# Kernel tuning notes

Measured on AMD Instinct MI355X. Metric: run time of the kernel, lower is better.

## Reference

```python
import jax, jax.numpy as jnp
import numpy as np
import math

HID = 128
NH = 8
HD = HID // NH
NL = 3
CLIP = 10.0
EPS = 1e-5

def _ln(x, g, b):
    mu = jnp.mean(x, axis=-1, keepdims=True)
    var = jnp.var(x, axis=-1, keepdims=True)
    return (x - mu) * jax.lax.rsqrt(var + EPS) * g + b

def _layer(h, e_bias1, e_gate2, g1, b1, wh, g2, b2, w1, w2):
    B, N, _ = h.shape
    h_in = h
    hn = _ln(h, g1, b1)
    qkv = hn @ wh                                   # (B,N,3H)
    q, k, v = jnp.split(qkv, 3, axis=-1)
    q = q.reshape(B, N, NH, HD).transpose(0, 2, 1, 3)  # (B,nh,N,hd)
    k = k.reshape(B, N, NH, HD).transpose(0, 2, 1, 3)
    v = v.reshape(B, N, NH, HD).transpose(0, 2, 1, 3)
    att = jnp.einsum('bhid,bhjd->bhij', q, k) * (1.0 / math.sqrt(HD))
    att = jax.nn.softmax(att + e_bias1, axis=-1) * e_gate2
    y = jnp.einsum('bhij,bhjd->bhid', att, v)
    y = y.transpose(0, 2, 1, 3).reshape(B, N, HID)
    z = _ln(y + h_in, g2, b2)
    mlp = jax.nn.relu(z @ w1) @ w2
    return mlp + y

def setup_inputs() -> dict:
    key = jax.random.key(0)
    ks = jax.random.split(key, 9)
    d = {
        'node_features': jax.random.normal(ks[0], (16, 256, 2), jnp.float32),
        'edge_features': jax.random.normal(ks[1], (16, 256, 256, 1), jnp.float32),
        'Wn': jax.random.normal(ks[2], (2, HID), jnp.float32) * 0.5,
        'We_in': jax.random.normal(ks[3], (1, HID), jnp.float32) * 0.1,
        'ln1_g': jnp.ones((NL, HID), jnp.float32),
        'ln1_b': jnp.zeros((NL, HID), jnp.float32),
        'Wh': jax.random.normal(ks[4], (NL, HID, 3 * HID), jnp.float32) * (1.0 / math.sqrt(HID)),
        'We': jax.random.normal(ks[5], (NL, HID, 2 * NH), jnp.float32) * (1.0 / math.sqrt(HID)),
        'ln2_g': jnp.ones((NL, HID), jnp.float32),
        'ln2_b': jnp.zeros((NL, HID), jnp.float32),
        'W1': jax.random.normal(ks[6], (NL, HID, 4 * HID), jnp.float32) * (1.0 / math.sqrt(HID)),
        'W2': jax.random.normal(ks[7], (NL, 4 * HID, HID), jnp.float32) * (1.0 / math.sqrt(4 * HID)),
        'Wdec': jax.random.normal(ks[8], (HID, 1), jnp.float32) * (1.0 / math.sqrt(HID)),
    }
    return d

def reference(node_features, edge_features, Wn, We_in, ln1_g, ln1_b, Wh, We, ln2_g, ln2_b, W1, W2, Wdec):
    h = node_features @ Wn                              # (B,N,H)
    e = edge_features @ We_in                           # (B,N,N,H)
    for i in range(NL):
        ee = e @ We[i]                                  # (B,N,N,2*nh)
        ee = ee.transpose(0, 3, 1, 2)                   # (B,2*nh,N,N)
        e1, e2 = ee[:, :NH], ee[:, NH:]
        h = _layer(h, e1, e2, ln1_g[i], ln1_b[i], Wh[i], ln2_g[i], ln2_b[i], W1[i], W2[i])
    out = h @ Wdec                                      # (B,N,1)
    out = CLIP * jnp.tanh(out / math.sqrt(HID))
    return out
```

## Files before the change

kernel.cpp:

```cpp
#include <hip/hip_runtime.h>
#include <math.h>

#define HID 128
#define NHEAD 8
#define NL 3
#define NS 256
#define ROWS 4096

typedef __attribute__((ext_vector_type(8))) short bf16x8;
typedef __attribute__((ext_vector_type(4))) float f32x4;

__device__ __forceinline__ float us2f(unsigned short s) { return __uint_as_float(((unsigned)s) << 16); }
__device__ __forceinline__ unsigned short f2b(float f) {
    unsigned u = __float_as_uint(f);
    return (unsigned short)((u + 0x7fff + ((u >> 16) & 1)) >> 16);
}

__global__ __launch_bounds__(256) void k_prep(
    const float* __restrict__ Wh, const float* __restrict__ W1, const float* __restrict__ W2,
    const float* __restrict__ We_in, const float* __restrict__ We,
    unsigned short* __restrict__ WhH, unsigned short* __restrict__ WhL,
    unsigned short* __restrict__ W1H, unsigned short* __restrict__ W1L,
    unsigned short* __restrict__ W2H, unsigned short* __restrict__ W2L,
    float* __restrict__ sbuf)
{
    int b = blockIdx.x, t = threadIdx.x;
    if (b == 528) {
        if (t < NL * 2 * NHEAD) {
            int l = t / (2 * NHEAD), j = t % (2 * NHEAD);
            float acc = 0.f;
            for (int c = 0; c < HID; ++c)
                acc += We_in[c] * We[(long)(l * HID + c) * (2 * NHEAD) + j];
            sbuf[t] = acc;
        }
        return;
    }
    const float* S; unsigned short *OH, *OL; int K, N, kt, nt;
    if (b < 144) {
        int l = b / 48, rem = b % 48; kt = rem & 3; nt = rem >> 2; K = 128; N = 384;
        S = Wh + (long)l * 128 * 384; OH = WhH + (long)l * 384 * 128; OL = WhL + (long)l * 384 * 128;
    } else if (b < 336) {
        int b2 = b - 144; int l = b2 / 64, rem = b2 % 64; kt = rem & 3; nt = rem >> 2; K = 128; N = 512;
        S = W1 + (long)l * 128 * 512; OH = W1H + (long)l * 512 * 128; OL = W1L + (long)l * 512 * 128;
    } else {
        int b2 = b - 336; int l = b2 / 64, rem = b2 % 64; kt = rem & 15; nt = rem >> 4; K = 512; N = 128;
        S = W2 + (long)l * 512 * 128; OH = W2H + (long)l * 128 * 512; OL = W2L + (long)l * 128 * 512;
    }
    __shared__ float sm[32][33];
    int i0 = t >> 5, j = t & 31;
#pragma unroll
    for (int p = 0; p < 4; ++p) {
        int i = i0 + p * 8;
        sm[i][j] = S[(long)(kt * 32 + i) * N + nt * 32 + j];
    }
    __syncthreads();
#pragma unroll
    for (int p = 0; p < 4; ++p) {
        int n = i0 + p * 8;
        float v = sm[j][n];
        unsigned short hh = f2b(v);
        long o = (long)(nt * 32 + n) * K + kt * 32 + j;
        OH[o] = hh; OL[o] = f2b(v - us2f(hh));
    }
}

__global__ __launch_bounds__(256) void k_embln(
    const float* __restrict__ nf, const float* __restrict__ Wn,
    const float* __restrict__ g, const float* __restrict__ b,
    float* __restrict__ h, unsigned short* __restrict__ oh, unsigned short* __restrict__ ol)
{
    int w = threadIdx.x >> 6, lane = threadIdx.x & 63;
    int row = blockIdx.x * 4 + w;
    int base = row * HID;
    float n0 = nf[2 * row], n1 = nf[2 * row + 1];
    float v0 = n0 * Wn[lane]      + n1 * Wn[HID + lane];
    float v1 = n0 * Wn[64 + lane] + n1 * Wn[HID + 64 + lane];
    h[base + lane] = v0; h[base + 64 + lane] = v1;
    float s = v0 + v1, s2 = v0 * v0 + v1 * v1;
#pragma unroll
    for (int o = 32; o; o >>= 1) { s += __shfl_xor(s, o); s2 += __shfl_xor(s2, o); }
    float mu  = s * (1.f / HID);
    float var = s2 * (1.f / HID) - mu * mu;
    float inv = rsqrtf(var + 1e-5f);
    float o0 = (v0 - mu) * inv * g[lane]      + b[lane];
    float o1 = (v1 - mu) * inv * g[64 + lane] + b[64 + lane];
    unsigned short h0 = f2b(o0), h1 = f2b(o1);
    oh[base + lane] = h0;       ol[base + lane] = f2b(o0 - us2f(h0));
    oh[base + 64 + lane] = h1;  ol[base + 64 + lane] = f2b(o1 - us2f(h1));
}

__global__ __launch_bounds__(256) void k_ln(const float* __restrict__ x,
                                            const float* __restrict__ x2,
                                            const float* __restrict__ g,
                                            const float* __restrict__ b,
                                            unsigned short* __restrict__ oh,
                                            unsigned short* __restrict__ ol) {
    int w = threadIdx.x >> 6, lane = threadIdx.x & 63;
    int row = blockIdx.x * 4 + w;
    int base = row * HID;
    float v0 = x[base + lane] + x2[base + lane];
    float v1 = x[base + 64 + lane] + x2[base + 64 + lane];
    float s = v0 + v1, s2 = v0 * v0 + v1 * v1;
#pragma unroll
    for (int o = 32; o; o >>= 1) { s += __shfl_xor(s, o); s2 += __shfl_xor(s2, o); }
    float mu  = s * (1.f / HID);
    float var = s2 * (1.f / HID) - mu * mu;
    float inv = rsqrtf(var + 1e-5f);
    float o0 = (v0 - mu) * inv * g[lane]      + b[lane];
    float o1 = (v1 - mu) * inv * g[64 + lane] + b[64 + lane];
    unsigned short h0 = f2b(o0), h1 = f2b(o1);
    oh[base + lane] = h0;       ol[base + lane] = f2b(o0 - us2f(h0));
    oh[base + 64 + lane] = h1;  ol[base + 64 + lane] = f2b(o1 - us2f(h1));
}

__global__ __launch_bounds__(256, 4) void k_gemm(
    const unsigned short* __restrict__ Ah, const unsigned short* __restrict__ Al,
    const unsigned short* __restrict__ WH, const unsigned short* __restrict__ WL,
    float* __restrict__ Cf, unsigned short* __restrict__ Ch, unsigned short* __restrict__ Cl,
    int Nc, int K, int mode)
{
    __shared__ unsigned short sAh[64 * 72], sAl[64 * 72], sWh[64 * 72], sWl[64 * 72];
    int t = threadIdx.x;
    int row0 = blockIdx.y * 64, col0 = blockIdx.x * 64;
    int w = t >> 6, lane = t & 63;
    int m = lane & 15, quad = lane >> 4;
    f32x4 acc[4];
#pragma unroll
    for (int i = 0; i < 4; ++i) acc[i] = (f32x4){0.f, 0.f, 0.f, 0.f};

    for (int ks = 0; ks < K; ks += 64) {
        if (ks) __syncthreads();
        int r = t >> 3, ck = t & 7;
#pragma unroll
        for (int p = 0; p < 2; ++p) {
            int rr = r + p * 32;
            long ga = (long)(row0 + rr) * K + ks + ck * 8;
            long wa = (long)(col0 + rr) * K + ks + ck * 8;
            *(uint4*)&sAh[rr * 72 + ck * 8] = *(const uint4*)&Ah[ga];
            *(uint4*)&sAl[rr * 72 + ck * 8] = *(const uint4*)&Al[ga];
            *(uint4*)&sWh[rr * 72 + ck * 8] = *(const uint4*)&WH[wa];
            *(uint4*)&sWl[rr * 72 + ck * 8] = *(const uint4*)&WL[wa];
        }
        __syncthreads();
#pragma unroll
        for (int c = 0; c < 2; ++c) {
            bf16x8 ah = *(const bf16x8*)&sAh[(w * 16 + m) * 72 + c * 32 + quad * 8];
            bf16x8 al = *(const bf16x8*)&sAl[(w * 16 + m) * 72 + c * 32 + quad * 8];
#pragma unroll
            for (int nt = 0; nt < 4; ++nt) {
                bf16x8 wh = *(const bf16x8*)&sWh[(nt * 16 + m) * 72 + c * 32 + quad * 8];
                bf16x8 wl = *(const bf16x8*)&sWl[(nt * 16 + m) * 72 + c * 32 + quad * 8];
                acc[nt] = __builtin_amdgcn_mfma_f32_16x16x32_bf16(ah, wh, acc[nt], 0, 0, 0);
                acc[nt] = __builtin_amdgcn_mfma_f32_16x16x32_bf16(ah, wl, acc[nt], 0, 0, 0);
                acc[nt] = __builtin_amdgcn_mfma_f32_16x16x32_bf16(al, wh, acc[nt], 0, 0, 0);
            }
        }
    }
#pragma unroll
    for (int nt = 0; nt < 4; ++nt) {
#pragma unroll
        for (int r = 0; r < 4; ++r) {
            int row = row0 + w * 16 + quad * 4 + r;
            int col = col0 + nt * 16 + m;
            float v = acc[nt][r];
            if (mode == 0) {
                Cf[(long)row * Nc + col] = v;
            } else {
                v = fmaxf(v, 0.f);
                unsigned short hh = f2b(v);
                Ch[(long)row * Nc + col] = hh;
                Cl[(long)row * Nc + col] = f2b(v - us2f(hh));
            }
        }
    }
}

__global__ __launch_bounds__(256, 3) void k_w2ln(
    const unsigned short* __restrict__ Ah, const unsigned short* __restrict__ Al,
    const unsigned short* __restrict__ WH, const unsigned short* __restrict__ WL,
    const float* __restrict__ yres, float* __restrict__ hout,
    const float* __restrict__ g, const float* __restrict__ b,
    unsigned short* __restrict__ oh, unsigned short* __restrict__ ol)
{
    __shared__ unsigned short sA[2][16 * 72];
    __shared__ unsigned short sW[2][128 * 72];
    int t = threadIdx.x;
    int row0 = blockIdx.x * 16;
    int w = t >> 6, lane = t & 63;
    int m = lane & 15, quad = lane >> 4;
    f32x4 acc[2];
    acc[0] = (f32x4){0.f,0.f,0.f,0.f}; acc[1] = (f32x4){0.f,0.f,0.f,0.f};

    for (int ks = 0; ks < 512; ks += 64) {
        if (ks) __syncthreads();
        {
            int pl = t >> 7, tt = t & 127;
            int r = tt >> 3, ck = tt & 7;
            const unsigned short* src = pl ? Al : Ah;
            *(uint4*)&sA[pl][r * 72 + ck * 8] = *(const uint4*)&src[(long)(row0 + r) * 512 + ks + ck * 8];
        }
        {
            int r0 = t >> 3, ck = t & 7;
#pragma unroll
            for (int p = 0; p < 4; ++p) {
                int n = r0 + p * 32;
                *(uint4*)&sW[0][n * 72 + ck * 8] = *(const uint4*)&WH[(long)n * 512 + ks + ck * 8];
                *(uint4*)&sW[1][n * 72 + ck * 8] = *(const uint4*)&WL[(long)n * 512 + ks + ck * 8];
            }
        }
        __syncthreads();
#pragma unroll
        for (int c = 0; c < 2; ++c) {
            bf16x8 ah = *(const bf16x8*)&sA[0][m * 72 + c * 32 + quad * 8];
            bf16x8 al = *(const bf16x8*)&sA[1][m * 72 + c * 32 + quad * 8];
#pragma unroll
            for (int nt = 0; nt < 2; ++nt) {
                int n = w * 32 + nt * 16 + m;
                bf16x8 wh = *(const bf16x8*)&sW[0][n * 72 + c * 32 + quad * 8];
                bf16x8 wl = *(const bf16x8*)&sW[1][n * 72 + c * 32 + quad * 8];
                acc[nt] = __builtin_amdgcn_mfma_f32_16x16x32_bf16(ah, wh, acc[nt], 0, 0, 0);
                acc[nt] = __builtin_amdgcn_mfma_f32_16x16x32_bf16(ah, wl, acc[nt], 0, 0, 0);
                acc[nt] = __builtin_amdgcn_mfma_f32_16x16x32_bf16(al, wh, acc[nt], 0, 0, 0);
            }
        }
    }
    __syncthreads();
    float* ht = (float*)&sW[0][0];
#pragma unroll
    for (int nt = 0; nt < 2; ++nt) {
#pragma unroll
        for (int r = 0; r < 4; ++r) {
            int row = quad * 4 + r;
            int col = w * 32 + nt * 16 + m;
            float v = acc[nt][r] + yres[(long)(row0 + row) * HID + col];
            hout[(long)(row0 + row) * HID + col] = v;
            ht[row * 132 + col] = v;
        }
    }
    __syncthreads();
    if (g) {
        int row = t >> 4, sub = t & 15;
        float v[8];
        *(float4*)&v[0] = *(const float4*)&ht[row * 132 + sub * 8];
        *(float4*)&v[4] = *(const float4*)&ht[row * 132 + sub * 8 + 4];
        float s = 0.f, s2 = 0.f;
#pragma unroll
        for (int j = 0; j < 8; ++j) { s += v[j]; s2 += v[j] * v[j]; }
        s  += __shfl_xor(s, 1);  s  += __shfl_xor(s, 2);  s  += __shfl_xor(s, 4);  s  += __shfl_xor(s, 8);
        s2 += __shfl_xor(s2, 1); s2 += __shfl_xor(s2, 2); s2 += __shfl_xor(s2, 4); s2 += __shfl_xor(s2, 8);
        float mu  = s * (1.f / HID);
        float var = s2 * (1.f / HID) - mu * mu;
        float inv = rsqrtf(var + 1e-5f);
        long base = (long)(row0 + row) * HID + sub * 8;
#pragma unroll
        for (int j = 0; j < 8; ++j) {
            int c = sub * 8 + j;
            float o = (v[j] - mu) * inv * g[c] + b[c];
            unsigned short hh = f2b(o);
            oh[base + j] = hh; ol[base + j] = f2b(o - us2f(hh));
        }
    }
}

__global__ __launch_bounds__(256) void k_attn(const float* __restrict__ qkv,
                                              const float* __restrict__ ef,
                                              const float* __restrict__ sbuf,
                                              int layer,
                                              float* __restrict__ y) {
    __shared__ float Ks[NS][20];
    __shared__ float Vt[16][NS + 4];
    __shared__ float Pb[4][4][NS];
    int bid = blockIdx.x;
    int q4 = bid & 3, hh = (bid >> 2) & 7, bb = bid >> 5;
    int t = threadIdx.x;
    {
        const float* kr = qkv + ((long)(bb * NS + t)) * 384 + HID + hh * 16;
        *(float4*)&Ks[t][0]  = *(const float4*)kr;
        *(float4*)&Ks[t][4]  = *(const float4*)(kr + 4);
        *(float4*)&Ks[t][8]  = *(const float4*)(kr + 8);
        *(float4*)&Ks[t][12] = *(const float4*)(kr + 12);
        const float* vr = kr + HID;
        float vv[16];
        *(float4*)&vv[0]  = *(const float4*)vr;
        *(float4*)&vv[4]  = *(const float4*)(vr + 4);
        *(float4*)&vv[8]  = *(const float4*)(vr + 8);
        *(float4*)&vv[12] = *(const float4*)(vr + 12);
#pragma unroll
        for (int d = 0; d < 16; ++d) Vt[d][t] = vv[d];
    }
    __syncthreads();
    int w = t >> 6, lane = t & 63;
    float s1  = sbuf[layer * 16 + hh];
    float s2g = sbuf[layer * 16 + NHEAD + hh];
    int part = lane >> 4, dd = lane & 15;
    for (int it = 0; it < 4; ++it) {
        int r0 = q4 * 64 + w * 16 + it * 4;
        float q[4][16];
#pragma unroll
        for (int rr = 0; rr < 4; ++rr) {
            const float* qr = qkv + ((long)(bb * NS + r0 + rr)) * 384 + hh * 16;
            *(float4*)&q[rr][0]  = *(const float4*)qr;
            *(float4*)&q[rr][4]  = *(const float4*)(qr + 4);
            *(float4*)&q[rr][8]  = *(const float4*)(qr + 8);
            *(float4*)&q[rr][12] = *(const float4*)(qr + 12);
        }
        float sc[4][4];
#pragma unroll
        for (int i = 0; i < 4; ++i) {
            int c = i * 64 + lane;
            float kk[16];
            *(float4*)&kk[0]  = *(const float4*)&Ks[c][0];
            *(float4*)&kk[4]  = *(const float4*)&Ks[c][4];
            *(float4*)&kk[8]  = *(const float4*)&Ks[c][8];
            *(float4*)&kk[12] = *(const float4*)&Ks[c][12];
#pragma unroll
            for (int rr = 0; rr < 4; ++rr) {
                float d0 = 0.f;
#pragma unroll
                for (int d = 0; d < 16; ++d) d0 += q[rr][d] * kk[d];
                sc[rr][i] = d0;
            }
        }
#pragma unroll
        for (int rr = 0; rr < 4; ++rr) {
            long eb = ((long)(bb * NS + r0 + rr)) * NS;
            float e0 = ef[eb + lane],       e1 = ef[eb + 64 + lane];
            float e2 = ef[eb + 128 + lane], e3 = ef[eb + 192 + lane];
            float x0 = sc[rr][0] * 0.25f + e0 * s1;
            float x1 = sc[rr][1] * 0.25f + e1 * s1;
            float x2 = sc[rr][2] * 0.25f + e2 * s1;
            float x3 = sc[rr][3] * 0.25f + e3 * s1;
            float m = fmaxf(fmaxf(x0, x1), fmaxf(x2, x3));
#pragma unroll
            for (int o = 32; o; o >>= 1) m = fmaxf(m, __shfl_xor(m, o));
            float p0 = __expf(x0 - m), p1 = __expf(x1 - m);
            float p2 = __expf(x2 - m), p3 = __expf(x3 - m);
            float sum = p0 + p1 + p2 + p3;
#pragma unroll
            for (int o = 32; o; o >>= 1) sum += __shfl_xor(sum, o);
            float inv = s2g / sum;
            Pb[w][rr][lane]       = p0 * inv * e0;
            Pb[w][rr][64 + lane]  = p1 * inv * e1;
            Pb[w][rr][128 + lane] = p2 * inv * e2;
            Pb[w][rr][192 + lane] = p3 * inv * e3;
        }
        float a0 = 0.f, a1 = 0.f, a2 = 0.f, a3 = 0.f;
#pragma unroll
        for (int ii = 0; ii < 16; ++ii) {
            int c = part * 64 + ((ii + part * 4) & 15) * 4;
            float4 vv = *(const float4*)&Vt[dd][c];
            float4 p;
            p = *(const float4*)&Pb[w][0][c]; a0 += vv.x*p.x + vv.y*p.y + vv.z*p.z + vv.w*p.w;
            p = *(const float4*)&Pb[w][1][c]; a1 += vv.x*p.x + vv.y*p.y + vv.z*p.z + vv.w*p.w;
            p = *(const float4*)&Pb[w][2][c]; a2 += vv.x*p.x + vv.y*p.y + vv.z*p.z + vv.w*p.w;
            p = *(const float4*)&Pb[w][3][c]; a3 += vv.x*p.x + vv.y*p.y + vv.z*p.z + vv.w*p.w;
        }
        a0 += __shfl_xor(a0, 16); a0 += __shfl_xor(a0, 32);
        a1 += __shfl_xor(a1, 16); a1 += __shfl_xor(a1, 32);
        a2 += __shfl_xor(a2, 16); a2 += __shfl_xor(a2, 32);
        a3 += __shfl_xor(a3, 16); a3 += __shfl_xor(a3, 32);
        if (lane < 16) {
            y[((long)(bb * NS + r0 + 0)) * HID + hh * 16 + dd] = a0;
            y[((long)(bb * NS + r0 + 1)) * HID + hh * 16 + dd] = a1;
            y[((long)(bb * NS + r0 + 2)) * HID + hh * 16 + dd] = a2;
            y[((long)(bb * NS + r0 + 3)) * HID + hh * 16 + dd] = a3;
        }
    }
}

__global__ __launch_bounds__(256) void k_dec(const float* __restrict__ h,
                                             const float* __restrict__ Wdec,
                                             float* __restrict__ out) {
    int w = threadIdx.x >> 6, lane = threadIdx.x & 63;
    int row = blockIdx.x * 4 + w;
    float a = h[(long)row * HID + lane] * Wdec[lane]
            + h[(long)row * HID + 64 + lane] * Wdec[64 + lane];
#pragma unroll
    for (int o = 32; o; o >>= 1) a += __shfl_xor(a, o);
    if (lane == 0) out[row] = 10.f * tanhf(a * 0.08838834764831845f);
}

extern "C" void kernel_launch(void* const* d_in, const int* in_sizes, int n_in,
                              void* d_out, int out_size, void* d_ws, size_t ws_size,
                              hipStream_t stream) {
    const float* nf    = (const float*)d_in[0];
    const float* ef    = (const float*)d_in[1];
    const float* Wn    = (const float*)d_in[2];
    const float* We_in = (const float*)d_in[3];
    const float* ln1g  = (const float*)d_in[4];
    const float* ln1b  = (const float*)d_in[5];
    const float* Wh    = (const float*)d_in[6];
    const float* We    = (const float*)d_in[7];
    const float* ln2g  = (const float*)d_in[8];
    const float* ln2b  = (const float*)d_in[9];
    const float* W1    = (const float*)d_in[10];
    const float* W2    = (const float*)d_in[11];
    const float* Wdec  = (const float*)d_in[12];

    float* ws   = (float*)d_ws;
    float* sbuf = ws;
    float* h    = ws + 64;
    float* y    = h + ROWS * HID;
    float* qkv  = y + ROWS * HID;
    unsigned short* hnH  = (unsigned short*)(qkv + (long)ROWS * 384);
    unsigned short* hnL  = hnH + (long)ROWS * HID;
    unsigned short* hidH = hnL + (long)ROWS * HID;
    unsigned short* hidL = hidH + (long)ROWS * 512;
    unsigned short* WhH  = hidL + (long)ROWS * 512;
    unsigned short* WhL  = WhH + (long)NL * 384 * 128;
    unsigned short* W1H  = WhL + (long)NL * 384 * 128;
    unsigned short* W1L  = W1H + (long)NL * 512 * 128;
    unsigned short* W2H  = W1L + (long)NL * 512 * 128;
    unsigned short* W2L  = W2H + (long)NL * 128 * 512;

    k_prep<<<529, 256, 0, stream>>>(Wh, W1, W2, We_in, We,
                                    WhH, WhL, W1H, W1L, W2H, W2L, sbuf);
    k_embln<<<ROWS / 4, 256, 0, stream>>>(nf, Wn, ln1g, ln1b, h, hnH, hnL);
    for (int l = 0; l < NL; ++l) {
        k_gemm<<<dim3(6, 64), 256, 0, stream>>>(hnH, hnL,
            WhH + (long)l * 384 * 128, WhL + (long)l * 384 * 128,
            qkv, nullptr, nullptr, 384, 128, 0);
        k_attn<<<512, 256, 0, stream>>>(qkv, ef, sbuf, l, y);
        k_ln<<<ROWS / 4, 256, 0, stream>>>(y, h, ln2g + l * HID, ln2b + l * HID, hnH, hnL);
        k_gemm<<<dim3(8, 64), 256, 0, stream>>>(hnH, hnL,
            W1H + (long)l * 512 * 128, W1L + (long)l * 512 * 128,
            nullptr, hidH, hidL, 512, 128, 1);
        int last = (l == NL - 1);
        k_w2ln<<<ROWS / 16, 256, 0, stream>>>(hidH, hidL,
            W2H + (long)l * 128 * 512, W2L + (long)l * 128 * 512,
            y, h,
            last ? nullptr : ln1g + (l + 1) * HID, last ? nullptr : ln1b + (l + 1) * HID,
            hnH, hnL);
    }
    k_dec<<<ROWS / 4, 256, 0, stream>>>(h, Wdec, (float*)d_out);
}
```

Baseline: 243.8 us.

## Fuse LayerNorm into GEMM prologue and decoder into final W2 epilogue

New measurement: 246.9 us. Within noise of the previous version (+1.3%).

```diff
diff --git a/kernel.cpp b/kernel.cpp
--- a/kernel.cpp
+++ b/kernel.cpp
@@ -19,12 +19,19 @@
 __global__ __launch_bounds__(256) void k_prep(
     const float* __restrict__ Wh, const float* __restrict__ W1, const float* __restrict__ W2,
     const float* __restrict__ We_in, const float* __restrict__ We,
+    const float* __restrict__ nf, const float* __restrict__ Wn,
     unsigned short* __restrict__ WhH, unsigned short* __restrict__ WhL,
     unsigned short* __restrict__ W1H, unsigned short* __restrict__ W1L,
     unsigned short* __restrict__ W2H, unsigned short* __restrict__ W2L,
-    float* __restrict__ sbuf)
+    float* __restrict__ sbuf, float* __restrict__ h)
 {
     int b = blockIdx.x, t = threadIdx.x;
+    if (b >= 529) {
+        int idx = (b - 529) * 256 + t;
+        int r = idx >> 7, c = idx & 127;
+        h[idx] = nf[2 * r] * Wn[c] + nf[2 * r + 1] * Wn[HID + c];
+        return;
+    }
     if (b == 528) {
         if (t < NL * 2 * NHEAD) {
             int l = t / (2 * NHEAD), j = t % (2 * NHEAD);
@@ -64,96 +71,78 @@
     }
 }
 
-__global__ __launch_bounds__(256) void k_embln(
-    const float* __restrict__ nf, const float* __restrict__ Wn,
+__global__ __launch_bounds__(256) void k_fgemm(
+    const float* __restrict__ x, const float* __restrict__ x2,
     const float* __restrict__ g, const float* __restrict__ b,
-    float* __restrict__ h, unsigned short* __restrict__ oh, unsigned short* __restrict__ ol)
-{
-    int w = threadIdx.x >> 6, lane = threadIdx.x & 63;
-    int row = blockIdx.x * 4 + w;
-    int base = row * HID;
-    float n0 = nf[2 * row], n1 = nf[2 * row + 1];
-    float v0 = n0 * Wn[lane]      + n1 * Wn[HID + lane];
-    float v1 = n0 * Wn[64 + lane] + n1 * Wn[HID + 64 + lane];
-    h[base + lane] = v0; h[base + 64 + lane] = v1;
-    float s = v0 + v1, s2 = v0 * v0 + v1 * v1;
-#pragma unroll
-    for (int o = 32; o; o >>= 1) { s += __shfl_xor(s, o); s2 += __shfl_xor(s2, o); }
-    float mu  = s * (1.f / HID);
-    float var = s2 * (1.f / HID) - mu * mu;
-    float inv = rsqrtf(var + 1e-5f);
-    float o0 = (v0 - mu) * inv * g[lane]      + b[lane];
-    float o1 = (v1 - mu) * inv * g[64 + lane] + b[64 + lane];
-    unsigned short h0 = f2b(o0), h1 = f2b(o1);
-    oh[base + lane] = h0;       ol[base + lane] = f2b(o0 - us2f(h0));
-    oh[base + 64 + lane] = h1;  ol[base + 64 + lane] = f2b(o1 - us2f(h1));
-}
-
-__global__ __launch_bounds__(256) void k_ln(const float* __restrict__ x,
-                                            const float* __restrict__ x2,
-                                            const float* __restrict__ g,
-                                            const float* __restrict__ b,
-                                            unsigned short* __restrict__ oh,
-                                            unsigned short* __restrict__ ol) {
-    int w = threadIdx.x >> 6, lane = threadIdx.x & 63;
-    int row = blockIdx.x * 4 + w;
-    int base = row * HID;
-    float v0 = x[base + lane] + x2[base + lane];
-    float v1 = x[base + 64 + lane] + x2[base + 64 + lane];
-    float s = v0 + v1, s2 = v0 * v0 + v1 * v1;
-#pragma unroll
-    for (int o = 32; o; o >>= 1) { s += __shfl_xor(s, o); s2 += __shfl_xor(s2, o); }
-    float mu  = s * (1.f / HID);
-    float var = s2 * (1.f / HID) - mu * mu;
-    float inv = rsqrtf(var + 1e-5f);
-    float o0 = (v0 - mu) * inv * g[lane]      + b[lane];
-    float o1 = (v1 - mu) * inv * g[64 + lane] + b[64 + lane];
-    unsigned short h0 = f2b(o0), h1 = f2b(o1);
-    oh[base + lane] = h0;       ol[base + lane] = f2b(o0 - us2f(h0));
-    oh[base + 64 + lane] = h1;  ol[base + 64 + lane] = f2b(o1 - us2f(h1));
-}
-
-__global__ __launch_bounds__(256, 4) void k_gemm(
-    const unsigned short* __restrict__ Ah, const unsigned short* __restrict__ Al,
     const unsigned short* __restrict__ WH, const unsigned short* __restrict__ WL,
     float* __restrict__ Cf, unsigned short* __restrict__ Ch, unsigned short* __restrict__ Cl,
-    int Nc, int K, int mode)
+    int Nc, int mode)
 {
-    __shared__ unsigned short sAh[64 * 72], sAl[64 * 72], sWh[64 * 72], sWl[64 * 72];
+    __shared__ unsigned short sAh[64 * 136], sAl[64 * 136];
+    __shared__ unsigned short sWh[64 * 136], sWl[64 * 136];
     int t = threadIdx.x;
     int row0 = blockIdx.y * 64, col0 = blockIdx.x * 64;
+
+#pragma unroll
+    for (int p = 0; p < 4; ++p) {
+        int rr = (t >> 4) + p * 16, ck = t & 15;
+        *(uint4*)&sWh[rr * 136 + ck * 8] = *(const uint4*)&WH[(long)(col0 + rr) * 128 + ck * 8];
+        *(uint4*)&sWl[rr * 136 + ck * 8] = *(const uint4*)&WL[(long)(col0 + rr) * 128 + ck * 8];
+    }
+#pragma unroll
+    for (int pass = 0; pass < 2; ++pass) {
+        int row = pass * 32 + (t >> 3);
+        int p = t & 7, cb = p * 16;
+        float v[16];
+        const float* xp = x + (long)(row0 + row) * HID + cb;
+#pragma unroll
+        for (int j = 0; j < 16; j += 4) *(float4*)&v[j] = *(const float4*)(xp + j);
+        if (x2) {
+            const float* yp = x2 + (long)(row0 + row) * HID + cb;
+#pragma unroll
+            for (int j = 0; j < 16; j += 4) {
+                float4 r4 = *(const float4*)(yp + j);
+                v[j] += r4.x; v[j+1] += r4.y; v[j+2] += r4.z; v[j+3] += r4.w;
+            }
+        }
+        float s = 0.f, s2 = 0.f;
+#pragma unroll
+        for (int j = 0; j < 16; ++j) { s += v[j]; s2 += v[j] * v[j]; }
+        s  += __shfl_xor(s, 1);  s  += __shfl_xor(s, 2);  s  += __shfl_xor(s, 4);
+        s2 += __shfl_xor(s2, 1); s2 += __shfl_xor(s2, 2); s2 += __shfl_xor(s2, 4);
+        float mu  = s * (1.f / HID);
+        float var = s2 * (1.f / HID) - mu * mu;
+        float inv = rsqrtf(var + 1e-5f);
+        unsigned short hi[16], lo[16];
+#pragma unroll
+        for (int j = 0; j < 16; ++j) {
+            int c = cb + j;
+            float o = (v[j] - mu) * inv * g[c] + b[c];
+            hi[j] = f2b(o); lo[j] = f2b(o - us2f(hi[j]));
+        }
+        *(uint4*)&sAh[row * 136 + cb]     = *(uint4*)&hi[0];
+        *(uint4*)&sAh[row * 136 + cb + 8] = *(uint4*)&hi[8];
+        *(uint4*)&sAl[row * 136 + cb]     = *(uint4*)&lo[0];
+        *(uint4*)&sAl[row * 136 + cb + 8] = *(uint4*)&lo[8];
+    }
+    __syncthreads();
+
     int w = t >> 6, lane = t & 63;
     int m = lane & 15, quad = lane >> 4;
     f32x4 acc[4];
 #pragma unroll
     for (int i = 0; i < 4; ++i) acc[i] = (f32x4){0.f, 0.f, 0.f, 0.f};
-
-    for (int ks = 0; ks < K; ks += 64) {
-        if (ks) __syncthreads();
-        int r = t >> 3, ck = t & 7;
-#pragma unroll
-        for (int p = 0; p < 2; ++p) {
-            int rr = r + p * 32;
-            long ga = (long)(row0 + rr) * K + ks + ck * 8;
-            long wa = (long)(col0 + rr) * K + ks + ck * 8;
-            *(uint4*)&sAh[rr * 72 + ck * 8] = *(const uint4*)&Ah[ga];
-            *(uint4*)&sAl[rr * 72 + ck * 8] = *(const uint4*)&Al[ga];
-            *(uint4*)&sWh[rr * 72 + ck * 8] = *(const uint4*)&WH[wa];
-            *(uint4*)&sWl[rr * 72 + ck * 8] = *(const uint4*)&WL[wa];
-        }
-        __syncthreads();
-#pragma unroll
-        for (int c = 0; c < 2; ++c) {
-            bf16x8 ah = *(const bf16x8*)&sAh[(w * 16 + m) * 72 + c * 32 + quad * 8];
-            bf16x8 al = *(const bf16x8*)&sAl[(w * 16 + m) * 72 + c * 32 + quad * 8];
-#pragma unroll
-            for (int nt = 0; nt < 4; ++nt) {
-                bf16x8 wh = *(const bf16x8*)&sWh[(nt * 16 + m) * 72 + c * 32 + quad * 8];
-                bf16x8 wl = *(const bf16x8*)&sWl[(nt * 16 + m) * 72 + c * 32 + quad * 8];
-                acc[nt] = __builtin_amdgcn_mfma_f32_16x16x32_bf16(ah, wh, acc[nt], 0, 0, 0);
-                acc[nt] = __builtin_amdgcn_mfma_f32_16x16x32_bf16(ah, wl, acc[nt], 0, 0, 0);
-                acc[nt] = __builtin_amdgcn_mfma_f32_16x16x32_bf16(al, wh, acc[nt], 0, 0, 0);
-            }
+#pragma unroll
+    for (int c = 0; c < 4; ++c) {
+        bf16x8 ah = *(const bf16x8*)&sAh[(w * 16 + m) * 136 + c * 32 + quad * 8];
+        bf16x8 al = *(const bf16x8*)&sAl[(w * 16 + m) * 136 + c * 32 + quad * 8];
+#pragma unroll
+        for (int nt = 0; nt < 4; ++nt) {
+            bf16x8 wh = *(const bf16x8*)&sWh[(nt * 16 + m) * 136 + c * 32 + quad * 8];
+            bf16x8 wl = *(const bf16x8*)&sWl[(nt * 16 + m) * 136 + c * 32 + quad * 8];
+            acc[nt] = __builtin_amdgcn_mfma_f32_16x16x32_bf16(ah, wh, acc[nt], 0, 0, 0);
+            acc[nt] = __builtin_amdgcn_mfma_f32_16x16x32_bf16(ah, wl, acc[nt], 0, 0, 0);
+            acc[nt] = __builtin_amdgcn_mfma_f32_16x16x32_bf16(al, wh, acc[nt], 0, 0, 0);
         }
     }
 #pragma unroll
@@ -179,8 +168,7 @@
     const unsigned short* __restrict__ Ah, const unsigned short* __restrict__ Al,
     const unsigned short* __restrict__ WH, const unsigned short* __restrict__ WL,
     const float* __restrict__ yres, float* __restrict__ hout,
-    const float* __restrict__ g, const float* __restrict__ b,
-    unsigned short* __restrict__ oh, unsigned short* __restrict__ ol)
+    const float* __restrict__ Wdec, float* __restrict__ out)
 {
     __shared__ unsigned short sA[2][16 * 72];
     __shared__ unsigned short sW[2][128 * 72];
@@ -238,27 +226,16 @@
         }
     }
     __syncthreads();
-    if (g) {
+    if (Wdec) {
         int row = t >> 4, sub = t & 15;
         float v[8];
         *(float4*)&v[0] = *(const float4*)&ht[row * 132 + sub * 8];
         *(float4*)&v[4] = *(const float4*)&ht[row * 132 + sub * 8 + 4];
-        float s = 0.f, s2 = 0.f;
-#pragma unroll
-        for (int j = 0; j < 8; ++j) { s += v[j]; s2 += v[j] * v[j]; }
-        s  += __shfl_xor(s, 1);  s  += __shfl_xor(s, 2);  s  += __shfl_xor(s, 4);  s  += __shfl_xor(s, 8);
-        s2 += __shfl_xor(s2, 1); s2 += __shfl_xor(s2, 2); s2 += __shfl_xor(s2, 4); s2 += __shfl_xor(s2, 8);
-        float mu  = s * (1.f / HID);
-        float var = s2 * (1.f / HID) - mu * mu;
-        float inv = rsqrtf(var + 1e-5f);
-        long base = (long)(row0 + row) * HID + sub * 8;
-#pragma unroll
-        for (int j = 0; j < 8; ++j) {
-            int c = sub * 8 + j;
-            float o = (v[j] - mu) * inv * g[c] + b[c];
-            unsigned short hh = f2b(o);
-            oh[base + j] = hh; ol[base + j] = f2b(o - us2f(hh));
-        }
+        float a = 0.f;
+#pragma unroll
+        for (int j = 0; j < 8; ++j) a += v[j] * Wdec[sub * 8 + j];
+        a += __shfl_xor(a, 1); a += __shfl_xor(a, 2); a += __shfl_xor(a, 4); a += __shfl_xor(a, 8);
+        if (sub == 0) out[row0 + row] = 10.f * tanhf(a * 0.08838834764831845f);
     }
 }
 
@@ -368,18 +345,6 @@
     }
 }
 
-__global__ __launch_bounds__(256) void k_dec(const float* __restrict__ h,
-                                             const float* __restrict__ Wdec,
-                                             float* __restrict__ out) {
-    int w = threadIdx.x >> 6, lane = threadIdx.x & 63;
-    int row = blockIdx.x * 4 + w;
-    float a = h[(long)row * HID + lane] * Wdec[lane]
-            + h[(long)row * HID + 64 + lane] * Wdec[64 + lane];
-#pragma unroll
-    for (int o = 32; o; o >>= 1) a += __shfl_xor(a, o);
-    if (lane == 0) out[row] = 10.f * tanhf(a * 0.08838834764831845f);
-}
-
 extern "C" void kernel_launch(void* const* d_in, const int* in_sizes, int n_in,
                               void* d_out, int out_size, void* d_ws, size_t ws_size,
                               hipStream_t stream) {
@@ -402,9 +367,7 @@
     float* h    = ws + 64;
     float* y    = h + ROWS * HID;
     float* qkv  = y + ROWS * HID;
-    unsigned short* hnH  = (unsigned short*)(qkv + (long)ROWS * 384);
-    unsigned short* hnL  = hnH + (long)ROWS * HID;
-    unsigned short* hidH = hnL + (long)ROWS * HID;
+    unsigned short* hidH = (unsigned short*)(qkv + (long)ROWS * 384);
     unsigned short* hidL = hidH + (long)ROWS * 512;
     unsigned short* WhH  = hidL + (long)ROWS * 512;
     unsigned short* WhL  = WhH + (long)NL * 384 * 128;
@@ -413,24 +376,21 @@
     unsigned short* W2H  = W1L + (long)NL * 512 * 128;
     unsigned short* W2L  = W2H + (long)NL * 128 * 512;
 
-    k_prep<<<529, 256, 0, stream>>>(Wh, W1, W2, We_in, We,
-                                    WhH, WhL, W1H, W1L, W2H, W2L, sbuf);
-    k_embln<<<ROWS / 4, 256, 0, stream>>>(nf, Wn, ln1g, ln1b, h, hnH, hnL);
+    k_prep<<<529 + ROWS * HID / 256, 256, 0, stream>>>(Wh, W1, W2, We_in, We, nf, Wn,
+                                    WhH, WhL, W1H, W1L, W2H, W2L, sbuf, h);
     for (int l = 0; l < NL; ++l) {
-        k_gemm<<<dim3(6, 64), 256, 0, stream>>>(hnH, hnL,
+        k_fgemm<<<dim3(6, 64), 256, 0, stream>>>(h, nullptr,
+            ln1g + l * HID, ln1b + l * HID,
             WhH + (long)l * 384 * 128, WhL + (long)l * 384 * 128,
-            qkv, nullptr, nullptr, 384, 128, 0);
+            qkv, nullptr, nullptr, 384, 0);
         k_attn<<<512, 256, 0, stream>>>(qkv, ef, sbuf, l, y);
-        k_ln<<<ROWS / 4, 256, 0, stream>>>(y, h, ln2g + l * HID, ln2b + l * HID, hnH, hnL);
-        k_gemm<<<dim3(8, 64), 256, 0, stream>>>(hnH, hnL,
+        k_fgemm<<<dim3(8, 64), 256, 0, stream>>>(y, h,
+            ln2g + l * HID, ln2b + l * HID,
             W1H + (long)l * 512 * 128, W1L + (long)l * 512 * 128,
-            nullptr, hidH, hidL, 512, 128, 1);
+            nullptr, hidH, hidL, 512, 1);
         int last = (l == NL - 1);
         k_w2ln<<<ROWS / 16, 256, 0, stream>>>(hidH, hidL,
             W2H + (long)l * 128 * 512, W2L + (long)l * 128 * 512,
-            y, h,
-            last ? nullptr : ln1g + (l + 1) * HID, last ? nullptr : ln1b + (l + 1) * HID,
-            hnH, hnL);
-    }
-    k_dec<<<ROWS / 4, 256, 0, stream>>>(h, Wdec, (float*)d_out);
-}
+            y, h, last ? Wdec : nullptr, (float*)d_out);
+    }
+}
```
